# Performance work log

Hardware: AMD Instinct MI355X
Metric: run time of the kernel (lower is better)

Reference implementation:

```python
import jax, jax.numpy as jnp
import numpy as np

SQ3 = 3.0 ** 0.5
SQ5 = 5.0 ** 0.5
SQ7 = 7.0 ** 0.5
C30 = (5.0 / 6.0) ** 0.5
C32 = (3.0 / 8.0) ** 0.5
EPS = 1e-12


def _sh_lmax3_component(vec):
    """e3nn o3.spherical_harmonics(lmax=3, normalize=True, normalization='component').

    vec: [E, 3] unnormalized edge vectors -> [E, 16] SH features.
    Follows e3nn's recursive polynomial evaluation (its 'norm' basis), then
    scales each l-block by sqrt(2l+1) for 'component' normalization.
    """
    r = jnp.sqrt(jnp.sum(vec * vec, axis=-1, keepdims=True))
    u = vec / jnp.maximum(r, EPS)  # normalize=True (F.normalize semantics)
    x, y, z = u[..., 0], u[..., 1], u[..., 2]

    sh_0_0 = jnp.ones_like(x)

    sh_1_0, sh_1_1, sh_1_2 = x, y, z

    sh_2_0 = SQ3 * x * z
    sh_2_1 = SQ3 * x * y
    y2 = y * y
    x2z2 = x * x + z * z
    sh_2_2 = y2 - 0.5 * x2z2
    sh_2_3 = SQ3 * y * z
    sh_2_4 = (SQ3 / 2.0) * (z * z - x * x)

    sh_3_0 = C30 * (sh_2_0 * z + sh_2_4 * x)
    sh_3_1 = SQ5 * sh_2_0 * y
    sh_3_2 = C32 * (4.0 * y2 - x2z2) * x
    sh_3_3 = 0.5 * y * (2.0 * y2 - 3.0 * x2z2)
    sh_3_4 = C32 * z * (4.0 * y2 - x2z2)
    sh_3_5 = SQ5 * sh_2_4 * y
    sh_3_6 = C30 * (sh_2_4 * z - sh_2_0 * x)

    # 'component' normalization: block l scaled by sqrt(2l+1)
    return jnp.stack(
        [
            sh_0_0,
            SQ3 * sh_1_0, SQ3 * sh_1_1, SQ3 * sh_1_2,
            SQ5 * sh_2_0, SQ5 * sh_2_1, SQ5 * sh_2_2, SQ5 * sh_2_3, SQ5 * sh_2_4,
            SQ7 * sh_3_0, SQ7 * sh_3_1, SQ7 * sh_3_2, SQ7 * sh_3_3,
            SQ7 * sh_3_4, SQ7 * sh_3_5, SQ7 * sh_3_6,
        ],
        axis=-1,
    )


def setup_inputs() -> dict:
    key = jax.random.key(0)
    k_pos, k_edge = jax.random.split(key)
    n_nodes, n_edges = 100000, 3200000
    pos = jax.random.normal(k_pos, (n_nodes, 3), dtype=jnp.float32)
    edge_index = jax.random.randint(k_edge, (2, n_edges), 0, n_nodes, dtype=jnp.int64)
    return {"pos": pos, "edge_index": edge_index}


def reference(pos, edge_index):
    # gather sender/receiver positions and form edge vectors
    edge_vectors = pos[edge_index[0]] - pos[edge_index[1]]  # [E, 3]
    edge_sh = _sh_lmax3_component(edge_vectors)  # [E, 16]
    return edge_sh
```

## Files before the change

kernel.cpp:

```cpp
#include <hip/hip_runtime.h>


#define SQ3f 1.7320508075688772f
#define SQ5f 2.2360679774997896f
#define SQ7f 2.6457513110645907f
#define C30f 0.9128709291752769f
#define C32f 0.6123724356957945f

typedef float f32x4 __attribute__((ext_vector_type(4)));

__global__ __launch_bounds__(256) void sh_edge_kernel(
    const float* __restrict__ pos,
    const int* __restrict__ eidx,
    f32x4* __restrict__ out4,
    int E)
{
    __shared__ float lds[256 * 16];

    const int t = threadIdx.x;
    const long long blk = blockIdx.x;
    const long long e = blk * 256 + t;

    if (e < E) {
        int s = eidx[e];
        int d = eidx[E + e];

        float vx = pos[3 * s + 0] - pos[3 * d + 0];
        float vy = pos[3 * s + 1] - pos[3 * d + 1];
        float vz = pos[3 * s + 2] - pos[3 * d + 2];

        float r2 = vx * vx + vy * vy + vz * vz;
        float r = sqrtf(r2);
        float inv = 1.0f / fmaxf(r, 1e-12f);

        float x = vx * inv;
        float y = vy * inv;
        float z = vz * inv;

        float x2 = x * x;
        float y2 = y * y;
        float z2 = z * z;
        float x2z2 = x2 + z2;

        float s20 = SQ3f * x * z;
        float s21 = SQ3f * x * y;
        float s22 = y2 - 0.5f * x2z2;
        float s23 = SQ3f * y * z;
        float s24 = 0.5f * SQ3f * (z2 - x2);

        float fy2 = 4.0f * y2 - x2z2;

        float s30 = C30f * (s20 * z + s24 * x);
        float s31 = SQ5f * s20 * y;
        float s32 = C32f * fy2 * x;
        float s33 = 0.5f * y * (2.0f * y2 - 3.0f * x2z2);
        float s34 = C32f * z * fy2;
        float s35 = SQ5f * s24 * y;
        float s36 = C30f * (s24 * z - s20 * x);

        float4 val[4];
        val[0] = make_float4(1.0f,        SQ3f * x,   SQ3f * y,   SQ3f * z);
        val[1] = make_float4(SQ5f * s20,  SQ5f * s21, SQ5f * s22, SQ5f * s23);
        val[2] = make_float4(SQ5f * s24,  SQ7f * s30, SQ7f * s31, SQ7f * s32);
        val[3] = make_float4(SQ7f * s33,  SQ7f * s34, SQ7f * s35, SQ7f * s36);

        #pragma unroll
        for (int q = 0; q < 4; ++q) {
            int col = q ^ ((t >> 1) & 3);
            *reinterpret_cast<float4*>(&lds[t * 16 + 4 * col]) = val[q];
        }
    }

    __syncthreads();

    const size_t base4 = (size_t)blk * 1024;
    const size_t total4 = (size_t)E * 4;
    #pragma unroll
    for (int j = 0; j < 4; ++j) {
        int k = j * 256 + t;
        int r = k >> 2;
        int qq = k & 3;
        int col = qq ^ ((r >> 1) & 3);
        f32x4 v = *reinterpret_cast<const f32x4*>(&lds[r * 16 + 4 * col]);
        size_t o = base4 + k;
        if (o < total4) {
            __builtin_nontemporal_store(v, &out4[o]);
        }
    }
}

extern "C" void kernel_launch(void* const* d_in, const int* in_sizes, int n_in,
                              void* d_out, int out_size, void* d_ws, size_t ws_size,
                              hipStream_t stream)
{
    const float* pos = (const float*)d_in[0];
    const int* eidx = (const int*)d_in[1];
    f32x4* out4 = (f32x4*)d_out;

    int E = in_sizes[1] / 2;
    int block = 256;
    int grid = (int)(((long long)E + block - 1) / block);
    sh_edge_kernel<<<grid, block, 0, stream>>>(pos, eidx, out4, E);
}
```

Baseline: 43.85 us.

## Use persistent grid-stride blocks with software-prefetched edge gathers

Replaces the one-tile-per-block launch with a persistent grid capped at 2048 blocks that strides over 256-edge tiles. Each block loads the indices and gathered positions for its next tile before the barrier and store phase of the current tile, so gather latency can overlap with the output writes. This removes per-block launch overhead and adds a second barrier per iteration. It also lowers the number of waves resident at once, which may reduce the memory-level parallelism a one-shot grid gets from many blocks.

```diff
diff --git a/kernel.cpp b/kernel.cpp
--- a/kernel.cpp
+++ b/kernel.cpp
@@ -9,83 +9,109 @@
 
 typedef float f32x4 __attribute__((ext_vector_type(4)));
 
+__device__ __forceinline__ void load_edge_vec(
+    const float* __restrict__ pos, const int* __restrict__ eidx,
+    long long tile, int t, int E,
+    float& vx, float& vy, float& vz)
+{
+    long long e = tile * 256 + t;
+    long long ec = (e < E) ? e : 0;
+    int s = eidx[ec];
+    int d = eidx[E + ec];
+    vx = pos[3 * s + 0] - pos[3 * d + 0];
+    vy = pos[3 * s + 1] - pos[3 * d + 1];
+    vz = pos[3 * s + 2] - pos[3 * d + 2];
+}
+
 __global__ __launch_bounds__(256) void sh_edge_kernel(
     const float* __restrict__ pos,
     const int* __restrict__ eidx,
     f32x4* __restrict__ out4,
-    int E)
+    int E, int nTiles)
 {
     __shared__ float lds[256 * 16];
 
     const int t = threadIdx.x;
-    const long long blk = blockIdx.x;
-    const long long e = blk * 256 + t;
+    const size_t total4 = (size_t)E * 4;
 
-    if (e < E) {
-        int s = eidx[e];
-        int d = eidx[E + e];
+    long long tile = blockIdx.x;
+    if (tile >= nTiles) return;
 
-        float vx = pos[3 * s + 0] - pos[3 * d + 0];
-        float vy = pos[3 * s + 1] - pos[3 * d + 1];
-        float vz = pos[3 * s + 2] - pos[3 * d + 2];
+    float vx, vy, vz;
+    load_edge_vec(pos, eidx, tile, t, E, vx, vy, vz);
 
-        float r2 = vx * vx + vy * vy + vz * vz;
-        float r = sqrtf(r2);
-        float inv = 1.0f / fmaxf(r, 1e-12f);
+    for (;;) {
+        long long e = tile * 256 + t;
+        if (e < E) {
+            float r2 = vx * vx + vy * vy + vz * vz;
+            float r = sqrtf(r2);
+            float inv = 1.0f / fmaxf(r, 1e-12f);
 
-        float x = vx * inv;
-        float y = vy * inv;
-        float z = vz * inv;
+            float x = vx * inv;
+            float y = vy * inv;
+            float z = vz * inv;
 
-        float x2 = x * x;
-        float y2 = y * y;
-        float z2 = z * z;
-        float x2z2 = x2 + z2;
+            float x2 = x * x;
+            float y2 = y * y;
+            float z2 = z * z;
+            float x2z2 = x2 + z2;
 
-        float s20 = SQ3f * x * z;
-        float s21 = SQ3f * x * y;
-        float s22 = y2 - 0.5f * x2z2;
-        float s23 = SQ3f * y * z;
-        float s24 = 0.5f * SQ3f * (z2 - x2);
+            float s20 = SQ3f * x * z;
+            float s21 = SQ3f * x * y;
+            float s22 = y2 - 0.5f * x2z2;
+            float s23 = SQ3f * y * z;
+            float s24 = 0.5f * SQ3f * (z2 - x2);
 
-        float fy2 = 4.0f * y2 - x2z2;
+            float fy2 = 4.0f * y2 - x2z2;
 
-        float s30 = C30f * (s20 * z + s24 * x);
-        float s31 = SQ5f * s20 * y;
-        float s32 = C32f * fy2 * x;
-        float s33 = 0.5f * y * (2.0f * y2 - 3.0f * x2z2);
-        float s34 = C32f * z * fy2;
-        float s35 = SQ5f * s24 * y;
-        float s36 = C30f * (s24 * z - s20 * x);
+            float s30 = C30f * (s20 * z + s24 * x);
+            float s31 = SQ5f * s20 * y;
+            float s32 = C32f * fy2 * x;
+            float s33 = 0.5f * y * (2.0f * y2 - 3.0f * x2z2);
+            float s34 = C32f * z * fy2;
+            float s35 = SQ5f * s24 * y;
+            float s36 = C30f * (s24 * z - s20 * x);
 
-        float4 val[4];
-        val[0] = make_float4(1.0f,        SQ3f * x,   SQ3f * y,   SQ3f * z);
-        val[1] = make_float4(SQ5f * s20,  SQ5f * s21, SQ5f * s22, SQ5f * s23);
-        val[2] = make_float4(SQ5f * s24,  SQ7f * s30, SQ7f * s31, SQ7f * s32);
-        val[3] = make_float4(SQ7f * s33,  SQ7f * s34, SQ7f * s35, SQ7f * s36);
+            float4 val[4];
+            val[0] = make_float4(1.0f,        SQ3f * x,   SQ3f * y,   SQ3f * z);
+            val[1] = make_float4(SQ5f * s20,  SQ5f * s21, SQ5f * s22, SQ5f * s23);
+            val[2] = make_float4(SQ5f * s24,  SQ7f * s30, SQ7f * s31, SQ7f * s32);
+            val[3] = make_float4(SQ7f * s33,  SQ7f * s34, SQ7f * s35, SQ7f * s36);
 
+            #pragma unroll
+            for (int q = 0; q < 4; ++q) {
+                int col = q ^ ((t >> 1) & 3);
+                *reinterpret_cast<float4*>(&lds[t * 16 + 4 * col]) = val[q];
+            }
+        }
+
+        long long next = tile + gridDim.x;
+        bool hasNext = (next < nTiles);
+        float nvx, nvy, nvz;
+        if (hasNext) {
+            load_edge_vec(pos, eidx, next, t, E, nvx, nvy, nvz);
+        }
+
+        __syncthreads();
+
+        const size_t base4 = (size_t)tile * 1024;
         #pragma unroll
-        for (int q = 0; q < 4; ++q) {
-            int col = q ^ ((t >> 1) & 3);
-            *reinterpret_cast<float4*>(&lds[t * 16 + 4 * col]) = val[q];
+        for (int i = 0; i < 4; ++i) {
+            int k = i * 256 + t;
+            int r = k >> 2;
+            int qq = k & 3;
+            int col = qq ^ ((r >> 1) & 3);
+            f32x4 v = *reinterpret_cast<const f32x4*>(&lds[r * 16 + 4 * col]);
+            size_t o = base4 + k;
+            if (o < total4) {
+                __builtin_nontemporal_store(v, &out4[o]);
+            }
         }
-    }
 
-    __syncthreads();
-
-    const size_t base4 = (size_t)blk * 1024;
-    const size_t total4 = (size_t)E * 4;
-    #pragma unroll
-    for (int j = 0; j < 4; ++j) {
-        int k = j * 256 + t;
-        int r = k >> 2;
-        int qq = k & 3;
-        int col = qq ^ ((r >> 1) & 3);
-        f32x4 v = *reinterpret_cast<const f32x4*>(&lds[r * 16 + 4 * col]);
-        size_t o = base4 + k;
-        if (o < total4) {
-            __builtin_nontemporal_store(v, &out4[o]);
-        }
+        if (!hasNext) break;
+        __syncthreads();
+        tile = next;
+        vx = nvx; vy = nvy; vz = nvz;
     }
 }
 
@@ -98,7 +124,7 @@
     f32x4* out4 = (f32x4*)d_out;
 
     int E = in_sizes[1] / 2;
-    int block = 256;
-    int grid = (int)(((long long)E + block - 1) / block);
-    sh_edge_kernel<<<grid, block, 0, stream>>>(pos, eidx, out4, E);
+    int nTiles = (int)(((long long)E + 255) / 256);
+    int grid = nTiles < 2048 ? nTiles : 2048;
+    sh_edge_kernel<<<grid, 256, 0, stream>>>(pos, eidx, out4, E, nTiles);
 }
```

Measured after the change: 46.05 us. 1.05x slower.
